# Optimization experiments

Measured on AMD Instinct MI355X. Metric: run time of the kernel, lower is better.

Reference implementation:

```python
import jax, jax.numpy as jnp
import numpy as np

D_MODEL = 1024
N_HEADS = 16
D_K = D_MODEL // N_HEADS


def setup_inputs() -> dict:
    key = jax.random.key(0)
    ks = jax.random.split(key, 9)
    s = 1.0 / np.sqrt(D_MODEL)
    x = jax.random.normal(ks[0], (2, 2048, D_MODEL), dtype=jnp.float32)
    Wq = jax.random.normal(ks[1], (D_MODEL, D_MODEL), dtype=jnp.float32) * s
    bq = jnp.zeros((D_MODEL,), jnp.float32)
    Wk = jax.random.normal(ks[2], (D_MODEL, D_MODEL), dtype=jnp.float32) * s
    bk = jnp.zeros((D_MODEL,), jnp.float32)
    Wv = jax.random.normal(ks[3], (D_MODEL, D_MODEL), dtype=jnp.float32) * s
    bv = jnp.zeros((D_MODEL,), jnp.float32)
    Wo = jax.random.normal(ks[4], (D_MODEL, D_MODEL), dtype=jnp.float32) * s
    bo = jnp.zeros((D_MODEL,), jnp.float32)
    return {"x": x, "Wq": Wq, "bq": bq, "Wk": Wk, "bk": bk,
            "Wv": Wv, "bv": bv, "Wo": Wo, "bo": bo}


def reference(x, Wq, bq, Wk, bk, Wv, bv, Wo, bo):
    B, T, C = x.shape
    H, Dk = N_HEADS, D_K
    # QKV projections, reshape to [B, H, T, Dk]
    q = (x @ Wq + bq).reshape(B, T, H, Dk).transpose(0, 2, 1, 3)
    k = (x @ Wk + bk).reshape(B, T, H, Dk).transpose(0, 2, 1, 3)
    v = (x @ Wv + bv).reshape(B, T, H, Dk).transpose(0, 2, 1, 3)
    scale = 1.0 / np.sqrt(Dk).astype(np.float32)
    att = jnp.einsum('bhqd,bhkd->bhqk', q, k) * scale  # [B,H,T,T]
    causal = jnp.tril(jnp.ones((T, T), dtype=bool))
    att = jnp.where(causal, att, -jnp.inf)
    att = jax.nn.softmax(att, axis=-1)
    y = jnp.einsum('bhqk,bhkd->bhqd', att, v)  # [B,H,T,Dk]
    y = y.transpose(0, 2, 1, 3).reshape(B, T, C)
    return y @ Wo + bo
```

## Files before the change

### kernel.cpp

```cpp
#include <hip/hip_runtime.h>
#include <stdint.h>

#define D_MODEL 1024
#define N_HEADS 16
#define D_K     64
#define T_SEQ   2048
#define BATCH   2
#define M_TOT   (BATCH * T_SEQ)
#define QCH     128
#define KVB     64

typedef __attribute__((ext_vector_type(8))) short  short8;
typedef __attribute__((ext_vector_type(4))) float  f32x4;
typedef __attribute__((ext_vector_type(4))) unsigned short u16x4;

typedef __attribute__((address_space(1))) void gvoid;
typedef __attribute__((address_space(3))) void lvoid;

#define QSCALE 0.18033688011112042f

static __device__ __forceinline__ unsigned short f2bf(float f) {
    union { float f; unsigned u; } v; v.f = f;
    unsigned u = v.u;
    u += 0x7fffu + ((u >> 16) & 1u);
    return (unsigned short)(u >> 16);
}
static __device__ __forceinline__ float bf2f(unsigned short s) {
    union { unsigned u; float f; } v; v.u = ((unsigned)s) << 16;
    return v.f;
}

__global__ void cvt_x(const float* __restrict__ in, unsigned short* __restrict__ out) {
    int idx = blockIdx.x * blockDim.x + threadIdx.x;
    const float4* in4 = (const float4*)in;
    float4 v = in4[idx];
    u16x4 o;
    o.x = f2bf(v.x); o.y = f2bf(v.y); o.z = f2bf(v.z); o.w = f2bf(v.w);
    *(u16x4*)&out[(size_t)idx * 4] = o;
}

__global__ void cvt_w_t(const float* w0, const float* w1, const float* w2, const float* w3,
                        unsigned short* o0, unsigned short* o1, unsigned short* o2, unsigned short* o3) {
    const float* w; unsigned short* o;
    switch (blockIdx.z) {
        case 0: w = w0; o = o0; break;
        case 1: w = w1; o = o1; break;
        case 2: w = w2; o = o2; break;
        default: w = w3; o = o3; break;
    }
    __shared__ float tile[32][33];
    int n0 = blockIdx.x * 32, k0 = blockIdx.y * 32;
    int tx = threadIdx.x, ty = threadIdx.y;
    #pragma unroll
    for (int r = 0; r < 32; r += 8)
        tile[ty + r][tx] = w[(size_t)(k0 + ty + r) * D_MODEL + n0 + tx];
    __syncthreads();
    #pragma unroll
    for (int r = 0; r < 32; r += 8)
        o[(size_t)(n0 + ty + r) * D_MODEL + k0 + tx] = f2bf(tile[tx][ty + r]);
}

__global__ __launch_bounds__(256) void gemm_qkv(const unsigned short* __restrict__ A,
                                                const unsigned short* __restrict__ wq,
                                                const unsigned short* __restrict__ wk,
                                                const unsigned short* __restrict__ wv,
                                                const float* __restrict__ bq,
                                                const float* __restrict__ bk,
                                                const float* __restrict__ bv,
                                                unsigned short* __restrict__ qo,
                                                unsigned short* __restrict__ ko,
                                                unsigned short* __restrict__ vo) {
    const int z = blockIdx.z;
    const unsigned short* Bt = (z == 0) ? wq : (z == 1) ? wk : wv;
    const float* bias = (z == 0) ? bq : (z == 1) ? bk : bv;
    const float alpha = (z == 0) ? QSCALE : 1.0f;

    __shared__ unsigned short lA[128 * 32];
    __shared__ unsigned short lB[128 * 32];
    const int tid  = threadIdx.x;
    const int w    = tid >> 6, lane = tid & 63;
    const int tm   = blockIdx.y, tn = blockIdx.x;
    const int wm   = w & 1, wn = w >> 1;
    const int i16  = lane & 15, g4 = lane >> 4;
    f32x4 acc[4][4] = {};

    const int rA0 = tm * 128, rB0 = tn * 128;
    const int srow = lane >> 2;
    const int skc  = (lane & 3) * 8;

    for (int k0 = 0; k0 < D_MODEL; k0 += 32) {
        #pragma unroll
        for (int is = 0; is < 2; ++is) {
            int c   = is * 4 + w;
            int row = c * 16 + srow;
            __builtin_amdgcn_global_load_lds(
                (gvoid*)(A + (size_t)(rA0 + row) * D_MODEL + k0 + skc),
                (lvoid*)&lA[c * 512], 16, 0, 0);
            __builtin_amdgcn_global_load_lds(
                (gvoid*)(Bt + (size_t)(rB0 + row) * D_MODEL + k0 + skc),
                (lvoid*)&lB[c * 512], 16, 0, 0);
        }
        __syncthreads();
        short8 af[4], bfr[4];
        #pragma unroll
        for (int mi = 0; mi < 4; ++mi)
            af[mi] = *(const short8*)&lA[(wm * 64 + mi * 16 + i16) * 32 + g4 * 8];
        #pragma unroll
        for (int ni = 0; ni < 4; ++ni)
            bfr[ni] = *(const short8*)&lB[(wn * 64 + ni * 16 + i16) * 32 + g4 * 8];
        #pragma unroll
        for (int mi = 0; mi < 4; ++mi)
            #pragma unroll
            for (int ni = 0; ni < 4; ++ni)
                acc[mi][ni] = __builtin_amdgcn_mfma_f32_16x16x32_bf16(af[mi], bfr[ni], acc[mi][ni], 0, 0, 0);
        __syncthreads();
    }

    #pragma unroll
    for (int mi = 0; mi < 4; ++mi)
        #pragma unroll
        for (int ni = 0; ni < 4; ++ni) {
            int col = tn * 128 + wn * 64 + ni * 16 + i16;
            float bv2 = bias[col];
            #pragma unroll
            for (int r = 0; r < 4; ++r) {
                int row = tm * 128 + wm * 64 + mi * 16 + g4 * 4 + r;
                float val = (acc[mi][ni][r] + bv2) * alpha;
                int b = row >> 11, t = row & (T_SEQ - 1);
                int h = col >> 6,  d = col & (D_K - 1);
                unsigned short bfv = f2bf(val);
                if (z == 2)
                    vo[(((size_t)(b * N_HEADS + h)) * D_K + d) * T_SEQ + t] = bfv;
                else if (z == 1)
                    ko[(((size_t)(b * N_HEADS + h)) * T_SEQ + t) * D_K + d] = bfv;
                else
                    qo[(((size_t)(b * N_HEADS + h)) * T_SEQ + t) * D_K + d] = bfv;
            }
        }
}

__global__ __launch_bounds__(256) void gemm_out(const unsigned short* __restrict__ A,
                                                const unsigned short* __restrict__ Bt,
                                                const float* __restrict__ bias,
                                                float* __restrict__ Cout) {
    __shared__ unsigned short lA[128 * 32];
    __shared__ unsigned short lB[128 * 32];
    const int tid  = threadIdx.x;
    const int w    = tid >> 6, lane = tid & 63;
    const int tm   = blockIdx.y, tn = blockIdx.x;
    const int wm   = w & 1, wn = w >> 1;
    const int i16  = lane & 15, g4 = lane >> 4;
    f32x4 acc[4][4] = {};

    const int rA0 = tm * 128, rB0 = tn * 128;
    const int srow = lane >> 2;
    const int skc  = (lane & 3) * 8;

    for (int k0 = 0; k0 < D_MODEL; k0 += 32) {
        #pragma unroll
        for (int is = 0; is < 2; ++is) {
            int c   = is * 4 + w;
            int row = c * 16 + srow;
            __builtin_amdgcn_global_load_lds(
                (gvoid*)(A + (size_t)(rA0 + row) * D_MODEL + k0 + skc),
                (lvoid*)&lA[c * 512], 16, 0, 0);
            __builtin_amdgcn_global_load_lds(
                (gvoid*)(Bt + (size_t)(rB0 + row) * D_MODEL + k0 + skc),
                (lvoid*)&lB[c * 512], 16, 0, 0);
        }
        __syncthreads();
        short8 af[4], bfr[4];
        #pragma unroll
        for (int mi = 0; mi < 4; ++mi)
            af[mi] = *(const short8*)&lA[(wm * 64 + mi * 16 + i16) * 32 + g4 * 8];
        #pragma unroll
        for (int ni = 0; ni < 4; ++ni)
            bfr[ni] = *(const short8*)&lB[(wn * 64 + ni * 16 + i16) * 32 + g4 * 8];
        #pragma unroll
        for (int mi = 0; mi < 4; ++mi)
            #pragma unroll
            for (int ni = 0; ni < 4; ++ni)
                acc[mi][ni] = __builtin_amdgcn_mfma_f32_16x16x32_bf16(af[mi], bfr[ni], acc[mi][ni], 0, 0, 0);
        __syncthreads();
    }

    #pragma unroll
    for (int mi = 0; mi < 4; ++mi)
        #pragma unroll
        for (int ni = 0; ni < 4; ++ni) {
            int col = tn * 128 + wn * 64 + ni * 16 + i16;
            float bv2 = bias[col];
            #pragma unroll
            for (int r = 0; r < 4; ++r) {
                int row = tm * 128 + wm * 64 + mi * 16 + g4 * 4 + r;
                Cout[(size_t)row * D_MODEL + col] = acc[mi][ni][r] + bv2;
            }
        }
}

__global__ __launch_bounds__(256, 4) void flash3(const unsigned short* __restrict__ q,
                                                 const unsigned short* __restrict__ k,
                                                 const unsigned short* __restrict__ vt,
                                                 unsigned short* __restrict__ opart,
                                                 float* __restrict__ lws) {
    __shared__ unsigned short lK[2][KVB * 64];
    __shared__ unsigned short lV[2][KVB * 64];
    __shared__ unsigned short lP[4][16 * 64];
    const int tid  = threadIdx.x;
    const int w    = tid >> 6, lane = tid & 63;
    const int i16  = lane & 15, g4 = lane >> 4;
    const int g8   = lane >> 3, l8 = lane & 7;
    const int bx   = blockIdx.x;
    const int c    = 15 - (bx >> 6);
    const int rem  = bx & 63;
    const int bh   = rem >> 1;
    const int half = rem & 1;
    const int q0w  = c * QCH + w * 32;
    const int t0   = half * (c + 1);

    const unsigned short* qp = q  + ((size_t)bh * T_SEQ + q0w) * D_K;
    const unsigned short* kp = k  + (size_t)bh * T_SEQ * D_K;
    const unsigned short* vp = vt + (size_t)bh * D_K * T_SEQ;
    unsigned short* Pw = &lP[w][0];

    const int swz  = (i16 & 7) << 3;
    const int csrc = (l8 ^ g8) << 3;

    short8 qf[2][2];
    #pragma unroll
    for (int qt = 0; qt < 2; ++qt)
        #pragma unroll
        for (int ks = 0; ks < 2; ++ks)
            qf[qt][ks] = *(const short8*)&qp[(qt * 16 + i16) * D_K + ks * 32 + g4 * 8];

    f32x4 o[2][4] = {};
    float l[2] = {0.f, 0.f};

    auto stage = [&](int buf, int kv0s) {
        #pragma unroll
        for (int i = 0; i < 2; ++i) {
            const int cidx = w * 2 + i;
            const int row  = cidx * 8 + g8;
            __builtin_amdgcn_global_load_lds(
                (gvoid*)(kp + (size_t)(kv0s + row) * D_K + csrc),
                (lvoid*)&lK[buf][cidx * 512], 16, 0, 0);
            __builtin_amdgcn_global_load_lds(
                (gvoid*)(vp + (size_t)row * T_SEQ + kv0s + csrc),
                (lvoid*)&lV[buf][cidx * 512], 16, 0, 0);
        }
    };

    stage(0, t0 * KVB);
    __syncthreads();

    for (int kvt = 0; kvt <= c; ++kvt) {
        const int cur = kvt & 1;
        const int kv0 = (t0 + kvt) * KVB;
        if (kvt < c) stage(cur ^ 1, kv0 + KVB);

        if (kv0 <= q0w + 31) {
            const bool act0 = (kv0 <= q0w + 15);
            f32x4 s[4][2] = {};
            __builtin_amdgcn_s_setprio(1);
            #pragma unroll
            for (int ks = 0; ks < 2; ++ks)
                #pragma unroll
                for (int kt = 0; kt < 4; ++kt) {
                    short8 ka = *(const short8*)&lK[cur][(kt * 16 + i16) * 64 + ((ks * 32 + g4 * 8) ^ swz)];
                    if (act0)
                        s[kt][0] = __builtin_amdgcn_mfma_f32_16x16x32_bf16(ka, qf[0][ks], s[kt][0], 0, 0, 0);
                    s[kt][1] = __builtin_amdgcn_mfma_f32_16x16x32_bf16(ka, qf[1][ks], s[kt][1], 0, 0, 0);
                }
            __builtin_amdgcn_s_setprio(0);
            #pragma unroll
            for (int qt = 0; qt < 2; ++qt) {
                if (qt == 0 && !act0) continue;
                const int qrow = q0w + qt * 16 + i16;
                const bool diag = (kv0 + KVB - 1 > q0w + qt * 16);
                float ps = 0.f;
                unsigned int pk[8];
                #pragma unroll
                for (int kt = 0; kt < 4; ++kt) {
                    f32x4 sc = s[kt][qt];
                    if (diag) {
                        #pragma unroll
                        for (int r = 0; r < 4; ++r)
                            if (kv0 + kt * 16 + g4 * 4 + r > qrow) sc[r] = -3e38f;
                    }
                    float p0 = exp2f(sc[0]), p1 = exp2f(sc[1]);
                    float p2 = exp2f(sc[2]), p3 = exp2f(sc[3]);
                    ps += (p0 + p1) + (p2 + p3);
                    pk[kt * 2]     = (unsigned)f2bf(p0) | ((unsigned)f2bf(p1) << 16);
                    pk[kt * 2 + 1] = (unsigned)f2bf(p2) | ((unsigned)f2bf(p3) << 16);
                }
                l[qt] += ps;
                #pragma unroll
                for (int kt = 0; kt < 4; ++kt) {
                    uint2 v2; v2.x = pk[kt * 2]; v2.y = pk[kt * 2 + 1];
                    *(uint2*)&Pw[i16 * 64 + ((kt * 16 + g4 * 4) ^ swz)] = v2;
                }
                short8 pB0 = *(const short8*)&Pw[i16 * 64 + (( 0 + g4 * 8) ^ swz)];
                short8 pB1 = *(const short8*)&Pw[i16 * 64 + ((32 + g4 * 8) ^ swz)];
                __builtin_amdgcn_s_setprio(1);
                #pragma unroll
                for (int dt = 0; dt < 4; ++dt) {
                    short8 va0 = *(const short8*)&lV[cur][(dt * 16 + i16) * 64 + (( 0 + g4 * 8) ^ swz)];
                    short8 va1 = *(const short8*)&lV[cur][(dt * 16 + i16) * 64 + ((32 + g4 * 8) ^ swz)];
                    o[qt][dt] = __builtin_amdgcn_mfma_f32_16x16x32_bf16(va0, pB0, o[qt][dt], 0, 0, 0);
                    o[qt][dt] = __builtin_amdgcn_mfma_f32_16x16x32_bf16(va1, pB1, o[qt][dt], 0, 0, 0);
                }
                __builtin_amdgcn_s_setprio(0);
            }
        }
        __syncthreads();
    }

    const int b = bh >> 4, h = bh & 15;
    unsigned short* op = opart + (size_t)half * ((size_t)M_TOT * D_MODEL);
    #pragma unroll
    for (int qt = 0; qt < 2; ++qt) {
        float lt = l[qt] + __shfl_xor(l[qt], 16);
        lt += __shfl_xor(lt, 32);
        const int trow = q0w + qt * 16 + i16;
        if (g4 == 0)
            lws[((size_t)half * 32 + bh) * T_SEQ + trow] = lt;
        #pragma unroll
        for (int dt = 0; dt < 4; ++dt) {
            u16x4 ov;
            ov.x = f2bf(o[qt][dt][0]);
            ov.y = f2bf(o[qt][dt][1]);
            ov.z = f2bf(o[qt][dt][2]);
            ov.w = f2bf(o[qt][dt][3]);
            *(u16x4*)&op[((size_t)(b * T_SEQ) + trow) * D_MODEL + h * D_K + dt * 16 + g4 * 4] = ov;
        }
    }
}

__global__ __launch_bounds__(256) void merge_halves(const unsigned short* __restrict__ op,
                                                    const float* __restrict__ lws,
                                                    unsigned short* __restrict__ y) {
    const int idx = blockIdx.x * 256 + threadIdx.x;
    const int gl  = idx * 8;
    const int row = gl >> 10;
    const int col = gl & 1023;
    const int b = row >> 11, t = row & (T_SEQ - 1), h = col >> 6;
    const float l0 = lws[((size_t)(b * 16 + h)) * T_SEQ + t];
    const float l1 = lws[((size_t)(32 + b * 16 + h)) * T_SEQ + t];
    const float inv = 1.0f / (l0 + l1);
    short8 a = *(const short8*)&op[gl];
    short8 cc = *(const short8*)&op[(size_t)M_TOT * D_MODEL + gl];
    short8 r;
    #pragma unroll
    for (int j = 0; j < 8; ++j) {
        float f = bf2f((unsigned short)a[j]) + bf2f((unsigned short)cc[j]);
        r[j] = (short)f2bf(f * inv);
    }
    *(short8*)&y[gl] = r;
}

extern "C" void kernel_launch(void* const* d_in, const int* in_sizes, int n_in,
                              void* d_out, int out_size, void* d_ws, size_t ws_size,
                              hipStream_t stream) {
    const float* x  = (const float*)d_in[0];
    const float* Wq = (const float*)d_in[1];
    const float* bq = (const float*)d_in[2];
    const float* Wk = (const float*)d_in[3];
    const float* bk = (const float*)d_in[4];
    const float* Wv = (const float*)d_in[5];
    const float* bv = (const float*)d_in[6];
    const float* Wo = (const float*)d_in[7];
    const float* bo = (const float*)d_in[8];

    uint8_t* ws = (uint8_t*)d_ws;
    const size_t MB = (size_t)1 << 20;
    unsigned short* xb  = (unsigned short*)(ws);
    unsigned short* wqt = (unsigned short*)(ws + 8  * MB);
    unsigned short* wkt = (unsigned short*)(ws + 10 * MB);
    unsigned short* wvt = (unsigned short*)(ws + 12 * MB);
    unsigned short* wot = (unsigned short*)(ws + 14 * MB);
    unsigned short* qb  = (unsigned short*)(ws + 16 * MB);
    unsigned short* kb  = (unsigned short*)(ws + 24 * MB);
    unsigned short* vtb = (unsigned short*)(ws + 32 * MB);
    float* lws = (float*)(ws + 8 * MB);

    cvt_x<<<4096, 256, 0, stream>>>(x, xb);
    cvt_w_t<<<dim3(32, 32, 4), dim3(32, 8), 0, stream>>>(Wq, Wk, Wv, Wo, wqt, wkt, wvt, wot);

    dim3 ggrid(D_MODEL / 128, M_TOT / 128, 3);
    gemm_qkv<<<ggrid, 256, 0, stream>>>(xb, wqt, wkt, wvt, bq, bk, bv, qb, kb, vtb);

    flash3<<<1024, 256, 0, stream>>>(qb, kb, vtb, (unsigned short*)d_out, lws);
    merge_halves<<<2048, 256, 0, stream>>>((const unsigned short*)d_out, lws, xb);

    gemm_out<<<dim3(D_MODEL / 128, M_TOT / 128), 256, 0, stream>>>(xb, wot, bo, (float*)d_out);
}
```

Measured before the change: 124.9 us.

## Pair causal query chunks per block, use 128-wide KV tiles, fast exp/bf16 pack

The attention kernel now gives each block two query chunks (c and 15-c) so causal work is balanced across blocks, and launches half as many blocks. KV is staged in 128-row tiles, and the two KV halves are interleaved as even/odd tiles rather than contiguous ranges. Softmax uses raw v_exp_f32 and v_cvt_pk_bf16_f32 inline asm in place of exp2f and manual rounding. The larger LDS footprint (about 72KB) and the removed occupancy hint may lower waves per CU, which could offset the gains from load balancing.

```diff
diff --git a/kernel.cpp b/kernel.cpp
--- a/kernel.cpp
+++ b/kernel.cpp
@@ -8,7 +8,6 @@
 #define BATCH   2
 #define M_TOT   (BATCH * T_SEQ)
 #define QCH     128
-#define KVB     64
 
 typedef __attribute__((ext_vector_type(8))) short  short8;
 typedef __attribute__((ext_vector_type(4))) float  f32x4;
@@ -28,6 +27,16 @@
 static __device__ __forceinline__ float bf2f(unsigned short s) {
     union { unsigned u; float f; } v; v.u = ((unsigned)s) << 16;
     return v.f;
+}
+static __device__ __forceinline__ float fexp2(float x) {
+    float r;
+    asm("v_exp_f32 %0, %1" : "=v"(r) : "v"(x));
+    return r;
+}
+static __device__ __forceinline__ unsigned cvt_pk_bf16(float lo, float hi) {
+    unsigned r;
+    asm("v_cvt_pk_bf16_f32 %0, %1, %2" : "=v"(r) : "v"(lo), "v"(hi));
+    return r;
 }
 
 __global__ void cvt_x(const float* __restrict__ in, unsigned short* __restrict__ out) {
@@ -198,140 +207,157 @@
         }
 }
 
-__global__ __launch_bounds__(256, 4) void flash3(const unsigned short* __restrict__ q,
-                                                 const unsigned short* __restrict__ k,
-                                                 const unsigned short* __restrict__ vt,
-                                                 unsigned short* __restrict__ opart,
-                                                 float* __restrict__ lws) {
-    __shared__ unsigned short lK[2][KVB * 64];
-    __shared__ unsigned short lV[2][KVB * 64];
+__global__ __launch_bounds__(256) void flash4(const unsigned short* __restrict__ q,
+                                              const unsigned short* __restrict__ k,
+                                              const unsigned short* __restrict__ vt,
+                                              unsigned short* __restrict__ opart,
+                                              float* __restrict__ lws) {
+    __shared__ unsigned short lK[2][128 * 64];
+    __shared__ unsigned short lV[2][64 * 128];
     __shared__ unsigned short lP[4][16 * 64];
     const int tid  = threadIdx.x;
     const int w    = tid >> 6, lane = tid & 63;
     const int i16  = lane & 15, g4 = lane >> 4;
-    const int g8   = lane >> 3, l8 = lane & 7;
+    const int l8   = lane & 7,  g8 = lane >> 3;
     const int bx   = blockIdx.x;
-    const int c    = 15 - (bx >> 6);
-    const int rem  = bx & 63;
-    const int bh   = rem >> 1;
-    const int half = rem & 1;
-    const int q0w  = c * QCH + w * 32;
-    const int t0   = half * (c + 1);
-
-    const unsigned short* qp = q  + ((size_t)bh * T_SEQ + q0w) * D_K;
+    const int h    = bx & 1;
+    const int bh   = (bx >> 1) & 31;
+    const int p    = bx >> 6;
+
     const unsigned short* kp = k  + (size_t)bh * T_SEQ * D_K;
     const unsigned short* vp = vt + (size_t)bh * D_K * T_SEQ;
     unsigned short* Pw = &lP[w][0];
-
     const int swz  = (i16 & 7) << 3;
-    const int csrc = (l8 ^ g8) << 3;
-
-    short8 qf[2][2];
-    #pragma unroll
-    for (int qt = 0; qt < 2; ++qt)
-        #pragma unroll
-        for (int ks = 0; ks < 2; ++ks)
-            qf[qt][ks] = *(const short8*)&qp[(qt * 16 + i16) * D_K + ks * 32 + g4 * 8];
-
-    f32x4 o[2][4] = {};
-    float l[2] = {0.f, 0.f};
-
-    auto stage = [&](int buf, int kv0s) {
-        #pragma unroll
-        for (int i = 0; i < 2; ++i) {
-            const int cidx = w * 2 + i;
-            const int row  = cidx * 8 + g8;
-            __builtin_amdgcn_global_load_lds(
-                (gvoid*)(kp + (size_t)(kv0s + row) * D_K + csrc),
-                (lvoid*)&lK[buf][cidx * 512], 16, 0, 0);
-            __builtin_amdgcn_global_load_lds(
-                (gvoid*)(vp + (size_t)row * T_SEQ + kv0s + csrc),
-                (lvoid*)&lV[buf][cidx * 512], 16, 0, 0);
+    const int ksrc = (l8 ^ g8) << 3;
+
+    const int b = bh >> 4, hh = bh & 15;
+    unsigned short* op = opart + (size_t)h * ((size_t)M_TOT * D_MODEL);
+
+    auto stage = [&](int buf, int t128) {
+        const int kvb = t128 * 128;
+        #pragma unroll
+        for (int i = 0; i < 4; ++i) {
+            const int ch  = w * 4 + i;
+            const int row = ch * 8 + g8;
+            __builtin_amdgcn_global_load_lds(
+                (gvoid*)(kp + (size_t)(kvb + row) * D_K + ksrc),
+                (lvoid*)&lK[buf][ch * 512], 16, 0, 0);
+        }
+        #pragma unroll
+        for (int i = 0; i < 4; ++i) {
+            const int ch  = w * 4 + i;
+            const int row = ch * 4 + (lane >> 4);
+            const int u   = (lane & 15) ^ (row & 7);
+            __builtin_amdgcn_global_load_lds(
+                (gvoid*)(vp + (size_t)row * T_SEQ + kvb + u * 8),
+                (lvoid*)&lV[buf][ch * 512], 16, 0, 0);
         }
     };
 
-    stage(0, t0 * KVB);
-    __syncthreads();
-
-    for (int kvt = 0; kvt <= c; ++kvt) {
-        const int cur = kvt & 1;
-        const int kv0 = (t0 + kvt) * KVB;
-        if (kvt < c) stage(cur ^ 1, kv0 + KVB);
-
-        if (kv0 <= q0w + 31) {
-            const bool act0 = (kv0 <= q0w + 15);
-            f32x4 s[4][2] = {};
-            __builtin_amdgcn_s_setprio(1);
+    #pragma unroll 1
+    for (int ci = 0; ci < 2; ++ci) {
+        const int c   = ci ? p : (15 - p);
+        const int q0w = c * QCH + w * 32;
+        const int cnt = (c >= h) ? ((c - h) >> 1) + 1 : 0;
+
+        const unsigned short* qp = q + ((size_t)bh * T_SEQ + q0w) * D_K;
+        short8 qf[2][2];
+        #pragma unroll
+        for (int qt = 0; qt < 2; ++qt)
             #pragma unroll
             for (int ks = 0; ks < 2; ++ks)
-                #pragma unroll
-                for (int kt = 0; kt < 4; ++kt) {
-                    short8 ka = *(const short8*)&lK[cur][(kt * 16 + i16) * 64 + ((ks * 32 + g4 * 8) ^ swz)];
-                    if (act0)
-                        s[kt][0] = __builtin_amdgcn_mfma_f32_16x16x32_bf16(ka, qf[0][ks], s[kt][0], 0, 0, 0);
-                    s[kt][1] = __builtin_amdgcn_mfma_f32_16x16x32_bf16(ka, qf[1][ks], s[kt][1], 0, 0, 0);
-                }
-            __builtin_amdgcn_s_setprio(0);
-            #pragma unroll
-            for (int qt = 0; qt < 2; ++qt) {
-                if (qt == 0 && !act0) continue;
-                const int qrow = q0w + qt * 16 + i16;
-                const bool diag = (kv0 + KVB - 1 > q0w + qt * 16);
-                float ps = 0.f;
-                unsigned int pk[8];
-                #pragma unroll
-                for (int kt = 0; kt < 4; ++kt) {
-                    f32x4 sc = s[kt][qt];
-                    if (diag) {
-                        #pragma unroll
-                        for (int r = 0; r < 4; ++r)
-                            if (kv0 + kt * 16 + g4 * 4 + r > qrow) sc[r] = -3e38f;
-                    }
-                    float p0 = exp2f(sc[0]), p1 = exp2f(sc[1]);
-                    float p2 = exp2f(sc[2]), p3 = exp2f(sc[3]);
-                    ps += (p0 + p1) + (p2 + p3);
-                    pk[kt * 2]     = (unsigned)f2bf(p0) | ((unsigned)f2bf(p1) << 16);
-                    pk[kt * 2 + 1] = (unsigned)f2bf(p2) | ((unsigned)f2bf(p3) << 16);
-                }
-                l[qt] += ps;
-                #pragma unroll
-                for (int kt = 0; kt < 4; ++kt) {
-                    uint2 v2; v2.x = pk[kt * 2]; v2.y = pk[kt * 2 + 1];
-                    *(uint2*)&Pw[i16 * 64 + ((kt * 16 + g4 * 4) ^ swz)] = v2;
-                }
-                short8 pB0 = *(const short8*)&Pw[i16 * 64 + (( 0 + g4 * 8) ^ swz)];
-                short8 pB1 = *(const short8*)&Pw[i16 * 64 + ((32 + g4 * 8) ^ swz)];
+                qf[qt][ks] = *(const short8*)&qp[(qt * 16 + i16) * D_K + ks * 32 + g4 * 8];
+
+        f32x4 o[2][4] = {};
+        float l[2] = {0.f, 0.f};
+
+        if (cnt > 0) stage(0, h);
+        __syncthreads();
+
+        for (int it = 0; it < cnt; ++it) {
+            const int cur = it & 1;
+            const int t   = h + 2 * it;
+            if (it + 1 < cnt) stage(cur ^ 1, t + 2);
+
+            #pragma unroll
+            for (int sub = 0; sub < 2; ++sub) {
+                const int kv0 = t * 128 + sub * 64;
+                if (kv0 > q0w + 31) continue;
+                const bool act0 = (kv0 <= q0w + 15);
+                const unsigned short* Kc = &lK[cur][sub * 64 * 64];
+
+                f32x4 s[4][2] = {};
                 __builtin_amdgcn_s_setprio(1);
                 #pragma unroll
-                for (int dt = 0; dt < 4; ++dt) {
-                    short8 va0 = *(const short8*)&lV[cur][(dt * 16 + i16) * 64 + (( 0 + g4 * 8) ^ swz)];
-                    short8 va1 = *(const short8*)&lV[cur][(dt * 16 + i16) * 64 + ((32 + g4 * 8) ^ swz)];
-                    o[qt][dt] = __builtin_amdgcn_mfma_f32_16x16x32_bf16(va0, pB0, o[qt][dt], 0, 0, 0);
-                    o[qt][dt] = __builtin_amdgcn_mfma_f32_16x16x32_bf16(va1, pB1, o[qt][dt], 0, 0, 0);
+                for (int ks = 0; ks < 2; ++ks)
+                    #pragma unroll
+                    for (int kt = 0; kt < 4; ++kt) {
+                        short8 ka = *(const short8*)&Kc[(kt * 16 + i16) * 64 + ((ks * 32 + g4 * 8) ^ swz)];
+                        if (act0)
+                            s[kt][0] = __builtin_amdgcn_mfma_f32_16x16x32_bf16(ka, qf[0][ks], s[kt][0], 0, 0, 0);
+                        s[kt][1] = __builtin_amdgcn_mfma_f32_16x16x32_bf16(ka, qf[1][ks], s[kt][1], 0, 0, 0);
+                    }
+                __builtin_amdgcn_s_setprio(0);
+
+                #pragma unroll
+                for (int qt = 0; qt < 2; ++qt) {
+                    if (qt == 0 && !act0) continue;
+                    const int qrow = q0w + qt * 16 + i16;
+                    const bool diag = (kv0 + 63 > q0w + qt * 16);
+                    float ps = 0.f;
+                    unsigned pk[8];
+                    #pragma unroll
+                    for (int kt = 0; kt < 4; ++kt) {
+                        f32x4 sc = s[kt][qt];
+                        if (diag) {
+                            #pragma unroll
+                            for (int r = 0; r < 4; ++r)
+                                if (kv0 + kt * 16 + g4 * 4 + r > qrow) sc[r] = -3e38f;
+                        }
+                        float p0 = fexp2(sc[0]), p1 = fexp2(sc[1]);
+                        float p2 = fexp2(sc[2]), p3 = fexp2(sc[3]);
+                        ps += (p0 + p1) + (p2 + p3);
+                        pk[kt * 2]     = cvt_pk_bf16(p0, p1);
+                        pk[kt * 2 + 1] = cvt_pk_bf16(p2, p3);
+                    }
+                    l[qt] += ps;
+                    #pragma unroll
+                    for (int kt = 0; kt < 4; ++kt) {
+                        uint2 v2; v2.x = pk[kt * 2]; v2.y = pk[kt * 2 + 1];
+                        *(uint2*)&Pw[i16 * 64 + ((kt * 16 + g4 * 4) ^ swz)] = v2;
+                    }
+                    short8 pB0 = *(const short8*)&Pw[i16 * 64 + (( 0 + g4 * 8) ^ swz)];
+                    short8 pB1 = *(const short8*)&Pw[i16 * 64 + ((32 + g4 * 8) ^ swz)];
+                    __builtin_amdgcn_s_setprio(1);
+                    #pragma unroll
+                    for (int dt = 0; dt < 4; ++dt) {
+                        short8 va0 = *(const short8*)&lV[cur][(dt * 16 + i16) * 128 + ((sub * 64 +  0 + g4 * 8) ^ swz)];
+                        short8 va1 = *(const short8*)&lV[cur][(dt * 16 + i16) * 128 + ((sub * 64 + 32 + g4 * 8) ^ swz)];
+                        o[qt][dt] = __builtin_amdgcn_mfma_f32_16x16x32_bf16(va0, pB0, o[qt][dt], 0, 0, 0);
+                        o[qt][dt] = __builtin_amdgcn_mfma_f32_16x16x32_bf16(va1, pB1, o[qt][dt], 0, 0, 0);
+                    }
+                    __builtin_amdgcn_s_setprio(0);
                 }
-                __builtin_amdgcn_s_setprio(0);
             }
-        }
-        __syncthreads();
-    }
-
-    const int b = bh >> 4, h = bh & 15;
-    unsigned short* op = opart + (size_t)half * ((size_t)M_TOT * D_MODEL);
-    #pragma unroll
-    for (int qt = 0; qt < 2; ++qt) {
-        float lt = l[qt] + __shfl_xor(l[qt], 16);
-        lt += __shfl_xor(lt, 32);
-        const int trow = q0w + qt * 16 + i16;
-        if (g4 == 0)
-            lws[((size_t)half * 32 + bh) * T_SEQ + trow] = lt;
-        #pragma unroll
-        for (int dt = 0; dt < 4; ++dt) {
-            u16x4 ov;
-            ov.x = f2bf(o[qt][dt][0]);
-            ov.y = f2bf(o[qt][dt][1]);
-            ov.z = f2bf(o[qt][dt][2]);
-            ov.w = f2bf(o[qt][dt][3]);
-            *(u16x4*)&op[((size_t)(b * T_SEQ) + trow) * D_MODEL + h * D_K + dt * 16 + g4 * 4] = ov;
+            __syncthreads();
+        }
+
+        #pragma unroll
+        for (int qt = 0; qt < 2; ++qt) {
+            float lt = l[qt] + __shfl_xor(l[qt], 16);
+            lt += __shfl_xor(lt, 32);
+            const int trow = q0w + qt * 16 + i16;
+            if (g4 == 0)
+                lws[((size_t)h * 32 + bh) * T_SEQ + trow] = lt;
+            #pragma unroll
+            for (int dt = 0; dt < 4; ++dt) {
+                u16x4 ov;
+                ov.x = f2bf(o[qt][dt][0]);
+                ov.y = f2bf(o[qt][dt][1]);
+                ov.z = f2bf(o[qt][dt][2]);
+                ov.w = f2bf(o[qt][dt][3]);
+                *(u16x4*)&op[((size_t)(b * T_SEQ) + trow) * D_MODEL + hh * D_K + dt * 16 + g4 * 4] = ov;
+            }
         }
     }
 }
@@ -389,7 +415,7 @@
     dim3 ggrid(D_MODEL / 128, M_TOT / 128, 3);
     gemm_qkv<<<ggrid, 256, 0, stream>>>(xb, wqt, wkt, wvt, bq, bk, bv, qb, kb, vtb);
 
-    flash3<<<1024, 256, 0, stream>>>(qb, kb, vtb, (unsigned short*)d_out, lws);
+    flash4<<<512, 256, 0, stream>>>(qb, kb, vtb, (unsigned short*)d_out, lws);
     merge_halves<<<2048, 256, 0, stream>>>((const unsigned short*)d_out, lws, xb);
 
     gemm_out<<<dim3(D_MODEL / 128, M_TOT / 128), 256, 0, stream>>>(xb, wot, bo, (float*)d_out);
```

Result: faster. 121.3 us (-2.9%).
